# Optimization experiments

Hardware: AMD Instinct MI355X
Metric: run time of the kernel (lower is better)

## Reference

```python
import jax, jax.numpy as jnp
import numpy as np
import math

S, B, F, H = 2048, 4, 512, 8
D = F // H  # head_dim = 64
THETA = 10000.0


def setup_inputs() -> dict:
    key = jax.random.key(0)
    ks = jax.random.split(key, 11)
    mk = lambda k, shape, scale=1.0: (jax.random.normal(k, shape, dtype=jnp.float32) * scale)
    s = 1.0 / math.sqrt(F)
    return {
        "q": mk(ks[0], (S, B, F)),
        "k": mk(ks[1], (S, B, F)),
        "v": mk(ks[2], (S, B, F)),
        "Wq": mk(ks[3], (F, F), s), "bq": mk(ks[4], (F,), s),
        "Wk": mk(ks[5], (F, F), s), "bk": mk(ks[6], (F,), s),
        "Wv": mk(ks[7], (F, F), s), "bv": mk(ks[8], (F,), s),
        "Wo": mk(ks[9], (F, F), s), "bo": mk(ks[10], (F,), s),
    }


def _to_batches(x):
    # (S, B, F) -> (B*H, S, D)
    return x.reshape(S, B, H, D).transpose(1, 2, 0, 3).reshape(B * H, S, D)


def _from_batches(y):
    # (B*H, S, D) -> (S, B, F)
    return y.reshape(B, H, S, D).transpose(2, 0, 1, 3).reshape(S, B, F)


def _rope(x):
    # interleaved RoPE on (B*H, S, D): pairs (even, odd) are (real, imag)
    xr = x.reshape(B * H, S, D // 2, 2)
    real, imag = xr[..., 0], xr[..., 1]
    thetas = THETA ** (-2.0 * jnp.arange(D // 2, dtype=jnp.float32) / D)  # (D/2,)
    ang = jnp.arange(S, dtype=jnp.float32)[:, None] * thetas[None, :]     # (S, D/2)
    cos, sin = jnp.cos(ang), jnp.sin(ang)
    even = real * cos - imag * sin
    odd = real * sin + imag * cos
    return jnp.stack([even, odd], axis=-1).reshape(B * H, S, D)


def reference(q, k, v, Wq, bq, Wk, bk, Wv, bv, Wo, bo):
    relu = jax.nn.relu
    q = relu(jnp.einsum('sbf,gf->sbg', q, Wq) + bq)
    k = relu(jnp.einsum('sbf,gf->sbg', k, Wk) + bk)
    v = relu(jnp.einsum('sbf,gf->sbg', v, Wv) + bv)
    q, k, v = _to_batches(q), _to_batches(k), _to_batches(v)
    q, k = _rope(q), _rope(k)
    scores = jnp.einsum('nqd,nkd->nqk', q, k) / math.sqrt(D)  # (B*H, S, S)
    attn = jax.nn.softmax(scores, axis=-1)
    y = jnp.einsum('nqk,nkd->nqd', attn, v)
    y = _from_batches(y)
    return relu(jnp.einsum('sbf,gf->sbg', y, Wo) + bo)
```

## Files before the change

### kernel.cpp

```cpp
#include <hip/hip_runtime.h>
#include <math.h>

#define S_LEN 2048
#define BATCH 4
#define FDIM 512
#define NHEAD 8
#define DHEAD 64

typedef unsigned short u16;
typedef short bf16x8 __attribute__((ext_vector_type(8)));
typedef float f32x4 __attribute__((ext_vector_type(4)));

__device__ __forceinline__ u16 f2bf(float f) {
    unsigned u = __float_as_uint(f);
    return (u16)((u + 0x7fffu + ((u >> 16) & 1u)) >> 16);
}
__device__ __forceinline__ ushort4 f2bf4(float4 t) {
    return (ushort4){f2bf(t.x), f2bf(t.y), f2bf(t.z), f2bf(t.w)};
}

__global__ __launch_bounds__(256) void gemm_qkv(
    const float* __restrict__ Aq, const float* __restrict__ Ak, const float* __restrict__ Av,
    const float* __restrict__ Wq, const float* __restrict__ Wk, const float* __restrict__ Wv,
    const float* __restrict__ bq, const float* __restrict__ bk, const float* __restrict__ bv,
    u16* __restrict__ Qb, u16* __restrict__ Kb, u16* __restrict__ Vtb, float qscale)
{
    __shared__ __align__(16) u16 pool[24576];
    const int tid = threadIdx.x;
    const int w = tid >> 6, lane = tid & 63;
    const int quad = lane >> 4, l16 = lane & 15;
    const int m0 = blockIdx.x * 128, n0 = blockIdx.y * 64, z = blockIdx.z;

    const float* A = (z == 0) ? Aq : (z == 1) ? Ak : Av;
    const float* W = (z == 0) ? Wq : (z == 1) ? Wk : Wv;
    const float* bias = (z == 0) ? bq : (z == 1) ? bk : bv;
    const float qs = (z == 0) ? qscale : 1.0f;

    const int srow = tid >> 4, scol = (tid & 15) * 4;

    f32x4 acc[2][4];
    #pragma unroll
    for (int rt = 0; rt < 2; rt++)
        #pragma unroll
        for (int nt = 0; nt < 4; nt++) acc[rt][nt] = (f32x4){0.f, 0.f, 0.f, 0.f};

    ushort4 ap[8], bp[4];
    auto loadT = [&](int k0) {
        #pragma unroll
        for (int it = 0; it < 8; it++) {
            int r = srow + it * 16;
            ap[it] = f2bf4(*(const float4*)(A + (size_t)(m0 + r) * FDIM + k0 + scol));
        }
        #pragma unroll
        for (int it = 0; it < 4; it++) {
            int r = srow + it * 16;
            bp[it] = f2bf4(*(const float4*)(W + (size_t)(n0 + r) * FDIM + k0 + scol));
        }
    };
    auto storeT = [&](int buf) {
        u16* Ab = pool + buf * 8192;
        u16* Bb = pool + 16384 + buf * 4096;
        #pragma unroll
        for (int it = 0; it < 8; it++) {
            int r = srow + it * 16;
            *(ushort4*)(Ab + r * 64 + (((scol >> 3) ^ (r & 7)) * 8) + (scol & 7)) = ap[it];
        }
        #pragma unroll
        for (int it = 0; it < 4; it++) {
            int r = srow + it * 16;
            *(ushort4*)(Bb + r * 64 + (((scol >> 3) ^ (r & 7)) * 8) + (scol & 7)) = bp[it];
        }
    };
    auto compute = [&](int buf) {
        const u16* Ab = pool + buf * 8192;
        const u16* Bb = pool + 16384 + buf * 4096;
        bf16x8 af[2][2];
        #pragma unroll
        for (int rt = 0; rt < 2; rt++) {
            const int row = w * 32 + rt * 16 + l16;
            af[rt][0] = *(const bf16x8*)(Ab + row * 64 + (((0 + quad) ^ (l16 & 7)) * 8));
            af[rt][1] = *(const bf16x8*)(Ab + row * 64 + (((4 + quad) ^ (l16 & 7)) * 8));
        }
        #pragma unroll
        for (int nt = 0; nt < 4; nt++) {
            const int rowb = nt * 16 + l16;
            bf16x8 b0 = *(const bf16x8*)(Bb + rowb * 64 + (((0 + quad) ^ (l16 & 7)) * 8));
            bf16x8 b1 = *(const bf16x8*)(Bb + rowb * 64 + (((4 + quad) ^ (l16 & 7)) * 8));
            #pragma unroll
            for (int rt = 0; rt < 2; rt++) {
                acc[rt][nt] = __builtin_amdgcn_mfma_f32_16x16x32_bf16(af[rt][0], b0, acc[rt][nt], 0, 0, 0);
                acc[rt][nt] = __builtin_amdgcn_mfma_f32_16x16x32_bf16(af[rt][1], b1, acc[rt][nt], 0, 0, 0);
            }
        }
    };

    loadT(0); storeT(0); __syncthreads();
    int cur = 0;
    #pragma unroll
    for (int i = 0; i < 8; i++) {
        if (i < 7) loadT((i + 1) * 64);
        compute(cur);
        if (i < 7) { storeT(1 - cur); cur = 1 - cur; __syncthreads(); }
    }

    float bvv[4];
    #pragma unroll
    for (int nt = 0; nt < 4; nt++) bvv[nt] = bias[n0 + nt * 16 + l16];
    const int h = blockIdx.y;
    u16* Epi = pool;

    if (z < 2) {
        u16* outB = (z == 0) ? Qb : Kb;
        const float NEG_LN1E4_32 = -0.2878231366242558f;
        float th[4];
        #pragma unroll
        for (int nt = 0; nt < 4; nt++)
            th[nt] = expf(NEG_LN1E4_32 * (float)(nt * 8 + (l16 >> 1)));
        #pragma unroll
        for (int pass = 0; pass < 2; pass++) {
            #pragma unroll
            for (int rt = 0; rt < 2; rt++) {
                const int s = (m0 >> 2) + w * 8 + rt * 4 + quad;
                #pragma unroll
                for (int nn = 0; nn < 2; nn++) {
                    const int nt = pass * 2 + nn;
                    float c, sn;
                    __sincosf((float)s * th[nt], &sn, &c);
                    #pragma unroll
                    for (int i = 0; i < 4; i++) {
                        float vv = fmaxf(acc[rt][nt][i] + bvv[nt], 0.f);
                        float t = __shfl_xor(vv, 1);
                        vv = (l16 & 1) ? (t * sn + vv * c) : (vv * c - t * sn);
                        Epi[(w * 32 + rt * 16 + quad * 4 + i) * 40 + nn * 16 + l16] = f2bf(vv * qs);
                    }
                }
            }
            asm volatile("s_waitcnt lgkmcnt(0)" ::: "memory");
            const int mloc = lane >> 1, seg = lane & 1;
            const int m = m0 + w * 32 + mloc;
            const int s2 = m >> 2, b = m & 3;
            const size_t dst = ((size_t)(b * 8 + h) * S_LEN + s2) * DHEAD + pass * 32 + seg * 16;
            uint4 t0 = *(const uint4*)&Epi[(w * 32 + mloc) * 40 + seg * 16];
            uint4 t1 = *(const uint4*)&Epi[(w * 32 + mloc) * 40 + seg * 16 + 8];
            *(uint4*)(outB + dst)     = t0;
            *(uint4*)(outB + dst + 8) = t1;
            asm volatile("s_waitcnt lgkmcnt(0)" ::: "memory");
        }
    } else {
        #pragma unroll
        for (int pass = 0; pass < 2; pass++) {
            #pragma unroll
            for (int rt = 0; rt < 2; rt++)
                #pragma unroll
                for (int nn = 0; nn < 2; nn++) {
                    const int nt = pass * 2 + nn;
                    #pragma unroll
                    for (int i = 0; i < 4; i++) {
                        float vv = fmaxf(acc[rt][nt][i] + bvv[nt], 0.f);
                        Epi[(w * 32 + rt * 16 + quad * 4 + i) * 40 + nn * 16 + l16] = f2bf(vv);
                    }
                }
            asm volatile("s_waitcnt lgkmcnt(0)" ::: "memory");
            const int half = lane >> 5, dp = lane & 31;
            const int d = pass * 32 + dp;
            const int sBase = (m0 >> 2) + w * 8;
            #pragma unroll
            for (int bb = 0; bb < 2; bb++) {
                const int b = half * 2 + bb;
                u16 tmp[8];
                #pragma unroll
                for (int sl = 0; sl < 8; sl++)
                    tmp[sl] = Epi[(w * 32 + sl * 4 + b) * 40 + dp];
                *(uint4*)(Vtb + ((size_t)(b * 8 + h) * DHEAD + d) * S_LEN + sBase) =
                    *(const uint4*)tmp;
            }
            asm volatile("s_waitcnt lgkmcnt(0)" ::: "memory");
        }
    }
}

__global__ __launch_bounds__(256) void gemm_out(
    const u16* __restrict__ A, const float* __restrict__ W,
    const float* __restrict__ bias, float* __restrict__ outF)
{
    __shared__ __align__(16) u16 pool[24576];
    const int tid = threadIdx.x;
    const int w = tid >> 6, lane = tid & 63;
    const int quad = lane >> 4, l16 = lane & 15;
    const int m0 = blockIdx.x * 128, n0 = blockIdx.y * 64;

    const int srow = tid >> 4, scol = (tid & 15) * 4;
    int rr[4], gg[4];
    #pragma unroll
    for (int it = 0; it < 4; it++) { int c = tid + it * 256; rr[it] = c >> 3; gg[it] = c & 7; }

    f32x4 acc[2][4];
    #pragma unroll
    for (int rt = 0; rt < 2; rt++)
        #pragma unroll
        for (int nt = 0; nt < 4; nt++) acc[rt][nt] = (f32x4){0.f, 0.f, 0.f, 0.f};

    uint4 av[4]; ushort4 bp[4];
    auto loadT = [&](int k0) {
        #pragma unroll
        for (int it = 0; it < 4; it++)
            av[it] = *(const uint4*)(A + (size_t)(m0 + rr[it]) * FDIM + k0 + gg[it] * 8);
        #pragma unroll
        for (int it = 0; it < 4; it++) {
            int r = srow + it * 16;
            bp[it] = f2bf4(*(const float4*)(W + (size_t)(n0 + r) * FDIM + k0 + scol));
        }
    };
    auto storeT = [&](int buf) {
        u16* Ab = pool + buf * 8192;
        u16* Bb = pool + 16384 + buf * 4096;
        #pragma unroll
        for (int it = 0; it < 4; it++)
            *(uint4*)(Ab + rr[it] * 64 + ((gg[it] ^ (rr[it] & 7)) * 8)) = av[it];
        #pragma unroll
        for (int it = 0; it < 4; it++) {
            int r = srow + it * 16;
            *(ushort4*)(Bb + r * 64 + (((scol >> 3) ^ (r & 7)) * 8) + (scol & 7)) = bp[it];
        }
    };
    auto compute = [&](int buf) {
        const u16* Ab = pool + buf * 8192;
        const u16* Bb = pool + 16384 + buf * 4096;
        bf16x8 af[2][2];
        #pragma unroll
        for (int rt = 0; rt < 2; rt++) {
            const int row = w * 32 + rt * 16 + l16;
            af[rt][0] = *(const bf16x8*)(Ab + row * 64 + (((0 + quad) ^ (l16 & 7)) * 8));
            af[rt][1] = *(const bf16x8*)(Ab + row * 64 + (((4 + quad) ^ (l16 & 7)) * 8));
        }
        #pragma unroll
        for (int nt = 0; nt < 4; nt++) {
            const int rowb = nt * 16 + l16;
            bf16x8 b0 = *(const bf16x8*)(Bb + rowb * 64 + (((0 + quad) ^ (l16 & 7)) * 8));
            bf16x8 b1 = *(const bf16x8*)(Bb + rowb * 64 + (((4 + quad) ^ (l16 & 7)) * 8));
            #pragma unroll
            for (int rt = 0; rt < 2; rt++) {
                acc[rt][nt] = __builtin_amdgcn_mfma_f32_16x16x32_bf16(af[rt][0], b0, acc[rt][nt], 0, 0, 0);
                acc[rt][nt] = __builtin_amdgcn_mfma_f32_16x16x32_bf16(af[rt][1], b1, acc[rt][nt], 0, 0, 0);
            }
        }
    };

    loadT(0); storeT(0); __syncthreads();
    int cur = 0;
    #pragma unroll
    for (int i = 0; i < 8; i++) {
        if (i < 7) loadT((i + 1) * 64);
        compute(cur);
        if (i < 7) { storeT(1 - cur); cur = 1 - cur; __syncthreads(); }
    }

    float bvv[4];
    #pragma unroll
    for (int nt = 0; nt < 4; nt++) bvv[nt] = bias[n0 + nt * 16 + l16];
    #pragma unroll
    for (int rt = 0; rt < 2; rt++)
        #pragma unroll
        for (int nt = 0; nt < 4; nt++)
            #pragma unroll
            for (int i = 0; i < 4; i++) {
                const int m = m0 + w * 32 + rt * 16 + quad * 4 + i;
                outF[(size_t)m * FDIM + n0 + nt * 16 + l16] =
                    fmaxf(acc[rt][nt][i] + bvv[nt], 0.f);
            }
}

__global__ __launch_bounds__(256, 4) void flash_attn_mfma(
    const u16* __restrict__ Q, const u16* __restrict__ K, const u16* __restrict__ Vt,
    float* __restrict__ Opart, float* __restrict__ Lpart)
{
    __shared__ __align__(16) u16 pool[16384];
    const int tid = threadIdx.x;
    const int w = tid >> 6, lane = tid & 63;
    const int quad = lane >> 4, l16 = lane & 15;
    const int s0 = blockIdx.x * 128, n = blockIdx.y, kh = blockIdx.z;

    const size_t baseQ = ((size_t)n * S_LEN + s0) * DHEAD;
    const size_t baseK = ((size_t)n * S_LEN + kh * 1024) * DHEAD;
    const size_t baseV = (size_t)n * DHEAD * S_LEN + kh * 1024;

    #pragma unroll
    for (int it = 0; it < 4; it++) {
        int c = tid + it * 256, r = c >> 3, g = c & 7;
        *(uint4*)(pool + r * 64 + ((g ^ (r & 7)) * 8)) =
            *(const uint4*)(Q + baseQ + r * DHEAD + g * 8);
    }
    __syncthreads();
    const int xa = ((0 + quad) ^ (l16 & 7)) * 8;
    const int xb = ((4 + quad) ^ (l16 & 7)) * 8;
    bf16x8 qa[2][2];
    #pragma unroll
    for (int s = 0; s < 2; s++) {
        const int row = w * 32 + s * 16 + l16;
        qa[s][0] = *(const bf16x8*)(pool + row * 64 + xa);
        qa[s][1] = *(const bf16x8*)(pool + row * 64 + xb);
    }
    __syncthreads();

    f32x4 accO[2][4];
    #pragma unroll
    for (int s = 0; s < 2; s++)
        #pragma unroll
        for (int dt = 0; dt < 4; dt++) accO[s][dt] = (f32x4){0.f, 0.f, 0.f, 0.f};
    float lsum[2] = {0.f, 0.f};

    const int sr = tid >> 3, sg = tid & 7;
    const int Hh = sg >> 2, vOff = ((sg >> 1) & 1) * 4;
    const int o1 = (2 * sg) & 3, o2 = (2 * sg + 1) & 3;
    uint4 kc[2], vc[2];
    auto loadKV = [&](int k0) {
        kc[0] = *(const uint4*)(K + baseK + (size_t)(k0 + sr) * DHEAD + sg * 8);
        kc[1] = *(const uint4*)(K + baseK + (size_t)(k0 + sr + 32) * DHEAD + sg * 8);
        vc[0] = *(const uint4*)(Vt + baseV + (size_t)sr * S_LEN + k0 + sg * 8);
        vc[1] = *(const uint4*)(Vt + baseV + (size_t)(sr + 32) * S_LEN + k0 + sg * 8);
    };
    auto storeKV = [&](int buf) {
        u16* Kb = pool + buf * 8192;
        u16* Vb = pool + 4096 + buf * 8192;
        const int swk = (sg ^ (sr & 7)) * 8;
        *(uint4*)(Kb + sr * 64 + swk)        = kc[0];
        *(uint4*)(Kb + (sr + 32) * 64 + swk) = kc[1];
        const int a1 = ((Hh * 4 + o1) ^ (sr & 7)) * 8 + vOff;
        const int a2 = ((Hh * 4 + o2) ^ (sr & 7)) * 8 + vOff;
        *(uint2*)(Vb + sr * 64 + a1)        = (uint2){vc[0].x, vc[0].y};
        *(uint2*)(Vb + sr * 64 + a2)        = (uint2){vc[0].z, vc[0].w};
        *(uint2*)(Vb + (sr + 32) * 64 + a1) = (uint2){vc[1].x, vc[1].y};
        *(uint2*)(Vb + (sr + 32) * 64 + a2) = (uint2){vc[1].z, vc[1].w};
    };

    loadKV(0);
    storeKV(0);
    __syncthreads();

    for (int i = 0; i < 16; i++) {
        const int buf = i & 1;
        const u16* Kbf = pool + buf * 8192;
        const u16* Vbf = pool + 4096 + buf * 8192;
        if (i < 15) loadKV((i + 1) * 64);

        f32x4 sc[2][4];
        #pragma unroll
        for (int kt = 0; kt < 4; kt++) {
            const int kr = kt * 16 + l16;
            bf16x8 kb0 = *(const bf16x8*)(Kbf + kr * 64 + xa);
            bf16x8 kb1 = *(const bf16x8*)(Kbf + kr * 64 + xb);
            #pragma unroll
            for (int s = 0; s < 2; s++) {
                f32x4 z = (f32x4){0.f, 0.f, 0.f, 0.f};
                z = __builtin_amdgcn_mfma_f32_16x16x32_bf16(kb0, qa[s][0], z, 0, 0, 0);
                z = __builtin_amdgcn_mfma_f32_16x16x32_bf16(kb1, qa[s][1], z, 0, 0, 0);
                sc[s][kt] = z;
            }
        }

        union { unsigned u[4]; bf16x8 v; } pb[2][2];
        #pragma unroll
        for (int s = 0; s < 2; s++) {
            unsigned dw[8];
            #pragma unroll
            for (int kt = 0; kt < 4; kt++) {
                float p0 = __builtin_amdgcn_exp2f(sc[s][kt][0] - 20.0f);
                float p1 = __builtin_amdgcn_exp2f(sc[s][kt][1] - 20.0f);
                float p2 = __builtin_amdgcn_exp2f(sc[s][kt][2] - 20.0f);
                float p3 = __builtin_amdgcn_exp2f(sc[s][kt][3] - 20.0f);
                dw[kt * 2 + 0] = __builtin_amdgcn_perm(__float_as_uint(p1), __float_as_uint(p0), 0x07060302u);
                dw[kt * 2 + 1] = __builtin_amdgcn_perm(__float_as_uint(p3), __float_as_uint(p2), 0x07060302u);
            }
            float a = 0.f;
            #pragma unroll
            for (int t = 0; t < 8; t++) {
                a += __uint_as_float(dw[t] << 16);
                a += __uint_as_float(dw[t] & 0xFFFF0000u);
            }
            lsum[s] += a;
            #pragma unroll
            for (int t = 0; t < 4; t++) { pb[s][0].u[t] = dw[t]; pb[s][1].u[t] = dw[4 + t]; }
        }

        #pragma unroll
        for (int dt = 0; dt < 4; dt++) {
            const int vr = dt * 16 + l16;
            bf16x8 va0 = *(const bf16x8*)(Vbf + vr * 64 + xa);
            bf16x8 va1 = *(const bf16x8*)(Vbf + vr * 64 + xb);
            #pragma unroll
            for (int s = 0; s < 2; s++) {
                accO[s][dt] = __builtin_amdgcn_mfma_f32_16x16x32_bf16(va0, pb[s][0].v, accO[s][dt], 0, 0, 0);
                accO[s][dt] = __builtin_amdgcn_mfma_f32_16x16x32_bf16(va1, pb[s][1].v, accO[s][dt], 0, 0, 0);
            }
        }

        if (i < 15) { storeKV(1 - buf); __syncthreads(); }
    }

    const int bI = n >> 3, h = n & 7;
    float* Ob = Opart + (size_t)kh * (8192 * 512);
    #pragma unroll
    for (int s = 0; s < 2; s++) {
        float l = lsum[s];
        l += __shfl_xor(l, 16);
        l += __shfl_xor(l, 32);
        const int qg = s0 + w * 32 + s * 16 + l16;
        if (quad == 0)
            Lpart[(size_t)kh * 65536 + n * 2048 + qg] = l;
        const size_t base = (size_t)(qg * BATCH + bI) * FDIM + h * DHEAD;
        #pragma unroll
        for (int dt = 0; dt < 4; dt++)
            *(float4*)(Ob + base + dt * 16 + quad * 4) =
                (float4){accO[s][dt][0], accO[s][dt][1], accO[s][dt][2], accO[s][dt][3]};
    }
}

__global__ __launch_bounds__(256) void combine_k(
    const float* __restrict__ O, const float* __restrict__ L, u16* __restrict__ Yb)
{
    const int idx = blockIdx.x * 256 + threadIdx.x;
    const int m = idx >> 7, c4 = idx & 127;
    const int g = c4 * 4, h = g >> 6;
    const int q = m >> 2, b = m & 3, n = b * 8 + h;
    const float l = L[n * 2048 + q] + L[65536 + n * 2048 + q];
    const float inv = 1.0f / l;
    const float4 o0 = *(const float4*)(O + (size_t)m * 512 + g);
    const float4 o1 = *(const float4*)(O + 4194304u + (size_t)m * 512 + g);
    ushort4 r = {f2bf((o0.x + o1.x) * inv), f2bf((o0.y + o1.y) * inv),
                 f2bf((o0.z + o1.z) * inv), f2bf((o0.w + o1.w) * inv)};
    *(ushort4*)(Yb + (size_t)m * 512 + g) = r;
}

extern "C" void kernel_launch(void* const* d_in, const int* in_sizes, int n_in,
                              void* d_out, int out_size, void* d_ws, size_t ws_size,
                              hipStream_t stream) {
    const float* q  = (const float*)d_in[0];
    const float* k  = (const float*)d_in[1];
    const float* v  = (const float*)d_in[2];
    const float* Wq = (const float*)d_in[3];
    const float* bq = (const float*)d_in[4];
    const float* Wk = (const float*)d_in[5];
    const float* bk = (const float*)d_in[6];
    const float* Wv = (const float*)d_in[7];
    const float* bv = (const float*)d_in[8];
    const float* Wo = (const float*)d_in[9];
    const float* bo = (const float*)d_in[10];
    float* out = (float*)d_out;

    const int NIN = S_LEN * BATCH * FDIM;
    u16* p = (u16*)d_ws;
    u16* Qb  = p;             p += NIN;
    u16* Kb  = p;             p += NIN;
    u16* Vtb = p;             p += NIN;
    float* Opart = (float*)p;
    float* Lpart = Opart + 2 * NIN;
    u16* Yb = Qb;

    const float QSCALE = 0.125f * 1.4426950408889634f;

    dim3 blk(256);
    dim3 gQKV(S_LEN * BATCH / 128, FDIM / 64, 3);
    gemm_qkv<<<gQKV, blk, 0, stream>>>(q, k, v, Wq, Wk, Wv, bq, bk, bv,
                                       Qb, Kb, Vtb, QSCALE);

    dim3 gAttn(S_LEN / 128, 32, 2);
    flash_attn_mfma<<<gAttn, blk, 0, stream>>>(Qb, Kb, Vtb, Opart, Lpart);

    combine_k<<<4096, blk, 0, stream>>>(Opart, Lpart, Yb);

    dim3 gOut(S_LEN * BATCH / 128, FDIM / 64);
    gemm_out<<<gOut, blk, 0, stream>>>(Yb, Wo, bo, out);
}
```

Baseline: 223.8 us.

## Fuse split-K attention combine into output GEMM and swap grid axes

Removes the separate combine kernel and folds the merge of the two partial attention outputs into the A-tile load of the output projection GEMM. Each tile sums the partials, normalizes by the summed row sums and converts to bf16. This saves one launch and the bf16 Y write and read. The QKV and output GEMM grids also swap axes so consecutive blocks walk the N dimension, which changes L2 reuse of the A rows. The cost is that the fp32 partials are read inside the GEMM load path, and each tile does more global traffic and ALU work per load.

New measurement: 263.5 us. +17.7%, slower.

```diff
diff --git a/kernel.cpp b/kernel.cpp
--- a/kernel.cpp
+++ b/kernel.cpp
@@ -29,7 +29,7 @@
     const int tid = threadIdx.x;
     const int w = tid >> 6, lane = tid & 63;
     const int quad = lane >> 4, l16 = lane & 15;
-    const int m0 = blockIdx.x * 128, n0 = blockIdx.y * 64, z = blockIdx.z;
+    const int m0 = blockIdx.y * 128, n0 = blockIdx.x * 64, z = blockIdx.z;
 
     const float* A = (z == 0) ? Aq : (z == 1) ? Ak : Av;
     const float* W = (z == 0) ? Wq : (z == 1) ? Wk : Wv;
@@ -106,7 +106,7 @@
     float bvv[4];
     #pragma unroll
     for (int nt = 0; nt < 4; nt++) bvv[nt] = bias[n0 + nt * 16 + l16];
-    const int h = blockIdx.y;
+    const int h = blockIdx.x;
     u16* Epi = pool;
 
     if (z < 2) {
@@ -180,14 +180,15 @@
 }
 
 __global__ __launch_bounds__(256) void gemm_out(
-    const u16* __restrict__ A, const float* __restrict__ W,
-    const float* __restrict__ bias, float* __restrict__ outF)
+    const float* __restrict__ Op, const float* __restrict__ Lp,
+    const float* __restrict__ W, const float* __restrict__ bias,
+    float* __restrict__ outF)
 {
     __shared__ __align__(16) u16 pool[24576];
     const int tid = threadIdx.x;
     const int w = tid >> 6, lane = tid & 63;
     const int quad = lane >> 4, l16 = lane & 15;
-    const int m0 = blockIdx.x * 128, n0 = blockIdx.y * 64;
+    const int m0 = blockIdx.y * 128, n0 = blockIdx.x * 64;
 
     const int srow = tid >> 4, scol = (tid & 15) * 4;
     int rr[4], gg[4];
@@ -201,10 +202,25 @@
         for (int nt = 0; nt < 4; nt++) acc[rt][nt] = (f32x4){0.f, 0.f, 0.f, 0.f};
 
     uint4 av[4]; ushort4 bp[4];
-    auto loadT = [&](int k0) {
-        #pragma unroll
-        for (int it = 0; it < 4; it++)
-            av[it] = *(const uint4*)(A + (size_t)(m0 + rr[it]) * FDIM + k0 + gg[it] * 8);
+    auto loadT = [&](int it8) {
+        const int k0 = it8 * 64;
+        #pragma unroll
+        for (int it = 0; it < 4; it++) {
+            const int r = rr[it], g = gg[it];
+            const int m = m0 + r, qq = m >> 2, b = m & 3;
+            const float invl = __builtin_amdgcn_rcpf(
+                Lp[(b * 8 + it8) * 2048 + qq] + Lp[65536 + (b * 8 + it8) * 2048 + qq]);
+            const float* o0 = Op + (size_t)m * 512 + k0 + g * 8;
+            const float* o1 = o0 + 4194304;
+            float4 a0 = *(const float4*)o0, a1 = *(const float4*)(o0 + 4);
+            float4 c0 = *(const float4*)o1, c1 = *(const float4*)(o1 + 4);
+            union { ushort s[8]; uint4 v; } pk;
+            pk.s[0] = f2bf((a0.x + c0.x) * invl); pk.s[1] = f2bf((a0.y + c0.y) * invl);
+            pk.s[2] = f2bf((a0.z + c0.z) * invl); pk.s[3] = f2bf((a0.w + c0.w) * invl);
+            pk.s[4] = f2bf((a1.x + c1.x) * invl); pk.s[5] = f2bf((a1.y + c1.y) * invl);
+            pk.s[6] = f2bf((a1.z + c1.z) * invl); pk.s[7] = f2bf((a1.w + c1.w) * invl);
+            av[it] = pk.v;
+        }
         #pragma unroll
         for (int it = 0; it < 4; it++) {
             int r = srow + it * 16;
@@ -250,7 +266,7 @@
     int cur = 0;
     #pragma unroll
     for (int i = 0; i < 8; i++) {
-        if (i < 7) loadT((i + 1) * 64);
+        if (i < 7) loadT(i + 1);
         compute(cur);
         if (i < 7) { storeT(1 - cur); cur = 1 - cur; __syncthreads(); }
     }
@@ -413,22 +429,6 @@
             *(float4*)(Ob + base + dt * 16 + quad * 4) =
                 (float4){accO[s][dt][0], accO[s][dt][1], accO[s][dt][2], accO[s][dt][3]};
     }
-}
-
-__global__ __launch_bounds__(256) void combine_k(
-    const float* __restrict__ O, const float* __restrict__ L, u16* __restrict__ Yb)
-{
-    const int idx = blockIdx.x * 256 + threadIdx.x;
-    const int m = idx >> 7, c4 = idx & 127;
-    const int g = c4 * 4, h = g >> 6;
-    const int q = m >> 2, b = m & 3, n = b * 8 + h;
-    const float l = L[n * 2048 + q] + L[65536 + n * 2048 + q];
-    const float inv = 1.0f / l;
-    const float4 o0 = *(const float4*)(O + (size_t)m * 512 + g);
-    const float4 o1 = *(const float4*)(O + 4194304u + (size_t)m * 512 + g);
-    ushort4 r = {f2bf((o0.x + o1.x) * inv), f2bf((o0.y + o1.y) * inv),
-                 f2bf((o0.z + o1.z) * inv), f2bf((o0.w + o1.w) * inv)};
-    *(ushort4*)(Yb + (size_t)m * 512 + g) = r;
 }
 
 extern "C" void kernel_launch(void* const* d_in, const int* in_sizes, int n_in,
@@ -454,20 +454,17 @@
     u16* Vtb = p;             p += NIN;
     float* Opart = (float*)p;
     float* Lpart = Opart + 2 * NIN;
-    u16* Yb = Qb;
 
     const float QSCALE = 0.125f * 1.4426950408889634f;
 
     dim3 blk(256);
-    dim3 gQKV(S_LEN * BATCH / 128, FDIM / 64, 3);
+    dim3 gQKV(FDIM / 64, S_LEN * BATCH / 128, 3);
     gemm_qkv<<<gQKV, blk, 0, stream>>>(q, k, v, Wq, Wk, Wv, bq, bk, bv,
                                        Qb, Kb, Vtb, QSCALE);
 
     dim3 gAttn(S_LEN / 128, 32, 2);
     flash_attn_mfma<<<gAttn, blk, 0, stream>>>(Qb, Kb, Vtb, Opart, Lpart);
 
-    combine_k<<<4096, blk, 0, stream>>>(Opart, Lpart, Yb);
-
-    dim3 gOut(S_LEN * BATCH / 128, FDIM / 64);
-    gemm_out<<<gOut, blk, 0, stream>>>(Yb, Wo, bo, out);
-}
+    dim3 gOut(FDIM / 64, S_LEN * BATCH / 128);
+    gemm_out<<<gOut, blk, 0, stream>>>(Opart, Lpart, Wo, bo, out);
+}
```
